# Optimization experiments

Measured on AMD Instinct MI355X. Metric: run time of the kernel, lower is better.

The kernel has to match this reference:

```python
import jax, jax.numpy as jnp
import numpy as np

B, L = 1024, 256
D = 64        # neighbor_interaction_feat_dim
TD = 100      # time_encoder.dim
NUM_NODES = 20000


def setup_inputs() -> dict:
    key = jax.random.key(0)
    ks = jax.random.split(key, 12)
    return {
        "src_ids": jax.random.randint(ks[0], (B, L), 0, NUM_NODES),
        "dst_ids": jax.random.randint(ks[1], (B, L), 0, NUM_NODES),
        "src_times": jax.random.uniform(ks[2], (B, L), jnp.float32),
        "dst_times": jax.random.uniform(ks[3], (B, L), jnp.float32),
        "node_times": jax.random.uniform(ks[4], (B,), jnp.float32) + 1.0,
        "num_nodes": NUM_NODES,
        # LTF time encoder: cos(t * w + b)
        "w_time": jax.random.normal(ks[5], (TD,), jnp.float32),
        "b_time": jax.random.normal(ks[6], (TD,), jnp.float32) * 0.1,
        # time_to_scalar: Linear(TD, 1)
        "w_ts": jax.random.normal(ks[7], (TD,), jnp.float32) / np.sqrt(TD),
        "b_ts": jnp.zeros((), jnp.float32),
        # MLP: Linear(1, D) -> ReLU -> Linear(D, D)
        "w1": jax.random.normal(ks[8], (D,), jnp.float32),
        "b1": jax.random.normal(ks[9], (D,), jnp.float32) * 0.1,
        "w2": jax.random.normal(ks[10], (D, D), jnp.float32) / np.sqrt(D),
        "b2": jax.random.normal(ks[11], (D,), jnp.float32) * 0.1,
    }


def _histogram(ids, num_nodes):
    # per-row count of each node id, with id==0 treated as padding (count 0)
    b = ids.shape[0]
    mask = (ids != 0).astype(jnp.float32)
    hist = jnp.zeros((b, num_nodes), jnp.float32)
    return hist.at[jnp.arange(b)[:, None], ids].add(mask)


def _time_weight(time_diff, w_time, b_time, w_ts, b_ts):
    # LTF: cos(t*w + b) -> Linear(TD,1) -> sigmoid, all fused elementwise+dot
    feat = jnp.cos(time_diff[..., None] * w_time + b_time)  # (B,L,TD)
    return jax.nn.sigmoid(feat @ w_ts + b_ts)               # (B,L)


def _mlp_sum(weighted_counts, w1, b1, w2, b2):
    # weighted_counts: (B,L,2) scalar counts -> Linear(1,D) -> ReLU -> Linear(D,D), sum over axis 2
    h = jax.nn.relu(weighted_counts[..., None] * w1 + b1)   # (B,L,2,D)
    return (h @ w2 + b2).sum(axis=2)                        # (B,L,D)


def reference(src_ids, dst_ids, src_times, dst_times, node_times, num_nodes,
              w_time, b_time, w_ts, b_ts, w1, b1, w2, b2):
    hist_src = _histogram(src_ids, num_nodes)  # (B,N)
    hist_dst = _histogram(dst_ids, num_nodes)

    c_ss = jnp.take_along_axis(hist_src, src_ids, axis=1)
    c_sd = jnp.take_along_axis(hist_dst, src_ids, axis=1)
    c_ds = jnp.take_along_axis(hist_src, dst_ids, axis=1)
    c_dd = jnp.take_along_axis(hist_dst, dst_ids, axis=1)

    src_counts = jnp.stack([c_ss, c_sd], axis=2)  # (B,L,2)
    dst_counts = jnp.stack([c_ds, c_dd], axis=2)

    src_w = _time_weight(node_times[:, None] - src_times, w_time, b_time, w_ts, b_ts)
    dst_w = _time_weight(node_times[:, None] - dst_times, w_time, b_time, w_ts, b_ts)

    src_features = _mlp_sum(src_counts * src_w[..., None], w1, b1, w2, b2)
    dst_features = _mlp_sum(dst_counts * dst_w[..., None], w1, b1, w2, b2)
    return src_features, dst_features
```

## Files before the change

kernel.cpp:

```cpp
#include <hip/hip_runtime.h>
#include <hip/hip_bf16.h>

#define BB 1024
#define LL 256
#define DD 64
#define TDIM 100

typedef _Float16 half8_t __attribute__((ext_vector_type(8)));
typedef float f32x4 __attribute__((ext_vector_type(4)));

__global__ __launch_bounds__(256, 2) void tni_kernel(
    const int* __restrict__ src_ids, const int* __restrict__ dst_ids,
    const float* __restrict__ src_tm, const float* __restrict__ dst_tm,
    const float* __restrict__ node_tm,
    const float* __restrict__ w_time, const float* __restrict__ b_time,
    const float* __restrict__ w_ts, const float* __restrict__ b_ts,
    const float* __restrict__ w1, const float* __restrict__ b1,
    const float* __restrict__ w2, const float* __restrict__ b2,
    float* __restrict__ out)
{
    __shared__ int4 ids_s4[LL/4];
    __shared__ int4 ids_d4[LL/4];
    __shared__ float wrv[TDIM], brv[TDIM], wtsv[TDIM];
    __shared__ float w1v[DD], b1v[DD];
    __shared__ half8_t W2v[DD*8];
    __shared__ half8_t Gv[LL*8];

    const int t    = threadIdx.x;
    const int b    = blockIdx.x >> 1;
    const int side = blockIdx.x & 1;

    ((int*)ids_s4)[t] = src_ids[b*LL + t];
    ((int*)ids_d4)[t] = dst_ids[b*LL + t];
    if (t < TDIM) {
        const float inv2pi = 0.15915494309189535f;
        wrv[t]  = w_time[t] * inv2pi;
        brv[t]  = b_time[t] * inv2pi;
        wtsv[t] = w_ts[t];
    }
    if (t < DD) {
        w1v[t] = w1[t];
        b1v[t] = b1[t];
    }
    {
        _Float16* w2s = (_Float16*)W2v;
        #pragma unroll
        for (int i = 0; i < 16; ++i) {
            int idx = t + 256*i;
            int e = idx >> 6, d = idx & 63;
            int chunk = (e >> 3) ^ (d & 7);
            w2s[d*64 + (chunk << 3) + (e & 7)] = (_Float16)w2[idx];
        }
    }
    __syncthreads();

    const int   my_id = side ? ((const int*)ids_d4)[t] : ((const int*)ids_s4)[t];
    const float my_tm = side ? dst_tm[b*LL + t] : src_tm[b*LL + t];

    int c1 = 0, c2 = 0;
    #pragma unroll 4
    for (int j = 0; j < LL/4; ++j) {
        int4 a  = ids_s4[j];
        int4 dd = ids_d4[j];
        c1 += (a.x==my_id) + (a.y==my_id) + (a.z==my_id) + (a.w==my_id);
        c2 += (dd.x==my_id) + (dd.y==my_id) + (dd.z==my_id) + (dd.w==my_id);
    }
    if (my_id == 0) { c1 = 0; c2 = 0; }

    float td = node_tm[b] - my_tm;
    float z  = b_ts[0];
    #pragma unroll 4
    for (int k = 0; k < TDIM; ++k) {
        float r = fmaf(td, wrv[k], brv[k]);
        r -= floorf(r);
        z = fmaf(__builtin_amdgcn_cosf(r), wtsv[k], z);
    }
    float ee  = __builtin_amdgcn_exp2f(-1.44269504f * z);
    float wgt = __builtin_amdgcn_rcpf(1.0f + ee);
    float c1w = (float)c1 * wgt;
    float c2w = (float)c2 * wgt;

    #pragma unroll
    for (int c = 0; c < 8; ++c) {
        half8_t h;
        #pragma unroll
        for (int j = 0; j < 8; ++j) {
            float w1e = w1v[c*8 + j], b1e = b1v[c*8 + j];
            float g = fmaxf(fmaf(c1w, w1e, b1e), 0.f)
                    + fmaxf(fmaf(c2w, w1e, b1e), 0.f);
            h[j] = (_Float16)g;
        }
        Gv[t*8 + (c ^ (t & 7))] = h;
    }
    __syncthreads();

    const int w    = t >> 6;
    const int l    = t & 63;
    const int quad = l >> 4;
    const int lr   = l & 15;

    f32x4 acc[4][4];
    #pragma unroll
    for (int mt = 0; mt < 4; ++mt)
        #pragma unroll
        for (int nt = 0; nt < 4; ++nt) {
            f32x4 zz = {0.f, 0.f, 0.f, 0.f};
            acc[mt][nt] = zz;
        }

    #pragma unroll
    for (int s = 0; s < 2; ++s) {
        const int c = s*4 + quad;
        half8_t bfr[4], afr[4];
        #pragma unroll
        for (int nt = 0; nt < 4; ++nt) {
            int n = nt*16 + lr;
            bfr[nt] = W2v[n*8 + (c ^ (n & 7))];
        }
        #pragma unroll
        for (int mt = 0; mt < 4; ++mt) {
            int row = w*64 + mt*16 + lr;
            afr[mt] = Gv[row*8 + (c ^ (row & 7))];
        }
        #pragma unroll
        for (int mt = 0; mt < 4; ++mt)
            #pragma unroll
            for (int nt = 0; nt < 4; ++nt)
                acc[mt][nt] = __builtin_amdgcn_mfma_f32_16x16x32_f16(
                    afr[mt], bfr[nt], acc[mt][nt], 0, 0, 0);
    }

    float b2v[4];
    #pragma unroll
    for (int nt = 0; nt < 4; ++nt)
        b2v[nt] = 2.f * b2[nt*16 + lr];

    const int obase = side * (BB*LL*DD) + b * (LL*DD);
    #pragma unroll
    for (int mt = 0; mt < 4; ++mt) {
        #pragma unroll
        for (int r = 0; r < 4; ++r) {
            int pos = w*64 + mt*16 + quad*4 + r;
            #pragma unroll
            for (int nt = 0; nt < 4; ++nt) {
                out[obase + pos*DD + nt*16 + lr] = acc[mt][nt][r] + b2v[nt];
            }
        }
    }
}

extern "C" void kernel_launch(void* const* d_in, const int* in_sizes, int n_in,
                              void* d_out, int out_size, void* d_ws, size_t ws_size,
                              hipStream_t stream) {
    const int* src_ids = (const int*)d_in[0];
    const int* dst_ids = (const int*)d_in[1];
    const float* src_tm  = (const float*)d_in[2];
    const float* dst_tm  = (const float*)d_in[3];
    const float* node_tm = (const float*)d_in[4];
    const float* w_time = (const float*)d_in[6];
    const float* b_time = (const float*)d_in[7];
    const float* w_ts   = (const float*)d_in[8];
    const float* b_ts   = (const float*)d_in[9];
    const float* w1     = (const float*)d_in[10];
    const float* b1     = (const float*)d_in[11];
    const float* w2     = (const float*)d_in[12];
    const float* b2     = (const float*)d_in[13];
    float* out = (float*)d_out;

    tni_kernel<<<dim3(BB*2), dim3(256), 0, stream>>>(
        src_ids, dst_ids, src_tm, dst_tm, node_tm,
        w_time, b_time, w_ts, b_ts, w1, b1, w2, b2, out);
}
```

Before: 176.0 us.

## Replace O(L) id comparison loop with shared-memory atomic histogram counting

```diff
diff --git a/kernel.cpp b/kernel.cpp
--- a/kernel.cpp
+++ b/kernel.cpp
@@ -1,10 +1,11 @@
 #include <hip/hip_runtime.h>
-#include <hip/hip_bf16.h>
 
 #define BB 1024
 #define LL 256
 #define DD 64
 #define TDIM 100
+#define NNODES 20000
+#define HWORDS ((NNODES + 1) / 2)
 
 typedef _Float16 half8_t __attribute__((ext_vector_type(8)));
 typedef float f32x4 __attribute__((ext_vector_type(4)));
@@ -19,19 +20,26 @@
     const float* __restrict__ w2, const float* __restrict__ b2,
     float* __restrict__ out)
 {
-    __shared__ int4 ids_s4[LL/4];
-    __shared__ int4 ids_d4[LL/4];
+    __shared__ unsigned int uS[10240];
     __shared__ float wrv[TDIM], brv[TDIM], wtsv[TDIM];
     __shared__ float w1v[DD], b1v[DD];
-    __shared__ half8_t W2v[DD*8];
-    __shared__ half8_t Gv[LL*8];
+
+    unsigned int* hist = uS;
+    half8_t* W2v = (half8_t*)uS;
+    half8_t* Gv  = (half8_t*)(uS + 2048);
 
     const int t    = threadIdx.x;
     const int b    = blockIdx.x >> 1;
     const int side = blockIdx.x & 1;
 
-    ((int*)ids_s4)[t] = src_ids[b*LL + t];
-    ((int*)ids_d4)[t] = dst_ids[b*LL + t];
+    const int   sid   = src_ids[b*LL + t];
+    const int   did   = dst_ids[b*LL + t];
+    const float my_tm = side ? dst_tm[b*LL + t] : src_tm[b*LL + t];
+
+    float w2r[16];
+    #pragma unroll
+    for (int i = 0; i < 16; ++i) w2r[i] = w2[t + 256*i];
+
     if (t < TDIM) {
         const float inv2pi = 0.15915494309189535f;
         wrv[t]  = w_time[t] * inv2pi;
@@ -42,30 +50,26 @@
         w1v[t] = w1[t];
         b1v[t] = b1[t];
     }
-    {
-        _Float16* w2s = (_Float16*)W2v;
-        #pragma unroll
-        for (int i = 0; i < 16; ++i) {
-            int idx = t + 256*i;
-            int e = idx >> 6, d = idx & 63;
-            int chunk = (e >> 3) ^ (d & 7);
-            w2s[d*64 + (chunk << 3) + (e & 7)] = (_Float16)w2[idx];
-        }
-    }
+
+    const int sw = sid >> 1, ssh = (sid & 1) * 16;
+    const int dw = did >> 1, dsh = (did & 1) * 16;
+    const int myw  = side ? dw  : sw;
+    const int mysh = side ? dsh : ssh;
+    const int my_id = side ? did : sid;
+
+    hist[sw] = 0; hist[dw] = 0;
     __syncthreads();
-
-    const int   my_id = side ? ((const int*)ids_d4)[t] : ((const int*)ids_s4)[t];
-    const float my_tm = side ? dst_tm[b*LL + t] : src_tm[b*LL + t];
-
-    int c1 = 0, c2 = 0;
-    #pragma unroll 4
-    for (int j = 0; j < LL/4; ++j) {
-        int4 a  = ids_s4[j];
-        int4 dd = ids_d4[j];
-        c1 += (a.x==my_id) + (a.y==my_id) + (a.z==my_id) + (a.w==my_id);
-        c2 += (dd.x==my_id) + (dd.y==my_id) + (dd.z==my_id) + (dd.w==my_id);
-    }
+    if (sid) atomicAdd(&hist[sw], 1u << ssh);
+    __syncthreads();
+    unsigned c1 = (hist[myw] >> mysh) & 0xffffu;
+    __syncthreads();
+    hist[sw] = 0; hist[dw] = 0;
+    __syncthreads();
+    if (did) atomicAdd(&hist[dw], 1u << dsh);
+    __syncthreads();
+    unsigned c2 = (hist[myw] >> mysh) & 0xffffu;
     if (my_id == 0) { c1 = 0; c2 = 0; }
+    __syncthreads();
 
     float td = node_tm[b] - my_tm;
     float z  = b_ts[0];
@@ -79,6 +83,17 @@
     float wgt = __builtin_amdgcn_rcpf(1.0f + ee);
     float c1w = (float)c1 * wgt;
     float c2w = (float)c2 * wgt;
+
+    {
+        _Float16* w2s = (_Float16*)W2v;
+        #pragma unroll
+        for (int i = 0; i < 16; ++i) {
+            int idx = t + 256*i;
+            int e = idx >> 6, d = idx & 63;
+            int chunk = (e >> 3) ^ (d & 7);
+            w2s[d*64 + (chunk << 3) + (e & 7)] = (_Float16)w2r[i];
+        }
+    }
 
     #pragma unroll
     for (int c = 0; c < 8; ++c) {
```

New measurement: 168.5 us. -4.3%, faster.
